# Kernel optimization log

Hardware: AMD Instinct MI355X
Metric: run time of the kernel (lower is better)

The kernel has to match this reference:

```python
import jax, jax.numpy as jnp
import numpy as np

S = 2048
HIDDEN = 4096
NH, NKV, HD = 32, 8, 128
QPK = NH // NKV  # 4
BLOCK, LOCAL, VERT = 64, 16, 8
ROPE_BASE = 1.0e6
SCALE = 1.0 / HD  # mup scaling: head_dim / mup_attn_multiplier(=1.0)


def setup_inputs() -> dict:
    key = jax.random.key(0)
    ks = jax.random.split(key, 5)
    qkv_out = NKV * (QPK + 2) * HD  # 6144, head-major layout
    return {
        "positions": jnp.arange(S, dtype=jnp.int32),
        "hidden_states": jax.random.normal(ks[0], (S, HIDDEN), jnp.float32),
        "w_qkv": jax.random.normal(ks[1], (qkv_out, HIDDEN), jnp.float32) * 0.02,
        "b_qkv": jax.random.normal(ks[2], (qkv_out,), jnp.float32) * 0.02,
        "w_dense": jax.random.normal(ks[3], (HIDDEN, HIDDEN), jnp.float32) * 0.02,
        "b_dense": jax.random.normal(ks[4], (HIDDEN,), jnp.float32) * 0.02,
    }


def _rope(x, cos, sin):
    # NeoX-style (non-interleaved) rotary over full head_dim.
    # x: [S, n_heads, HD]; cos/sin: [S, HD//2]
    d2 = x.shape[-1] // 2
    x1, x2 = x[..., :d2], x[..., d2:]
    c, s = cos[:, None, :], sin[:, None, :]
    return jnp.concatenate([x1 * c - x2 * s, x2 * c + x1 * s], axis=-1)


def _blocksparse_mask(positions):
    # vllm phi3small pattern: block (qb,kb) active iff causal AND
    # (qb-kb < local_blocks OR (kb + head + 1) % vert_stride == 0), hetero heads.
    qb = positions // BLOCK                       # [S]
    heads = jnp.arange(NH, dtype=positions.dtype)
    diff = qb[:, None] - qb[None, :]              # [S,S]
    local = diff < LOCAL                          # [S,S]
    vert = ((qb[None, None, :] + heads[:, None, None] + 1) % VERT) == 0  # [NH,1,S]
    causal = positions[:, None] >= positions[None, :]                     # [S,S]
    return (local[None] | vert) & causal[None]    # [NH,S,S]


def reference(positions, hidden_states, w_qkv, b_qkv, w_dense, b_dense):
    seq = hidden_states.shape[0]
    qkv = hidden_states @ w_qkv.T + b_qkv                   # [S, 6144]
    qkv = qkv.reshape(seq, NKV, QPK + 2, HD)                # head-major split
    q = qkv[:, :, :QPK].reshape(seq, NH, HD)
    k = qkv[:, :, QPK]                                      # [S, NKV, HD]
    v = qkv[:, :, QPK + 1]

    pos = positions.astype(jnp.float32)  # rope_position_scale = 1.0
    inv_freq = 1.0 / (ROPE_BASE ** (jnp.arange(0, HD, 2, dtype=jnp.float32) / HD))
    freqs = pos[:, None] * inv_freq                          # [S, HD/2]
    cos, sin = jnp.cos(freqs), jnp.sin(freqs)
    q = _rope(q, cos, sin)
    k = _rope(k, cos, sin)

    # GQA: each kv head serves QPK query heads
    kx = jnp.repeat(k, QPK, axis=1)                          # [S, NH, HD]
    vx = jnp.repeat(v, QPK, axis=1)

    scores = jnp.einsum('qhd,khd->hqk', q, kx) * SCALE       # [NH,S,S]
    mask = _blocksparse_mask(positions)
    scores = jnp.where(mask, scores, -jnp.inf)  # diag always in local block -> no empty rows
    p = jax.nn.softmax(scores, axis=-1)
    out = jnp.einsum('hqk,khd->qhd', p, vx).reshape(seq, NH * HD)
    return out @ w_dense.T + b_dense
```

## Files before the change

### kernel.cpp

```cpp
#include <hip/hip_runtime.h>

#define S_LEN   2048
#define HID     4096
#define NHEADS  32
#define NKVH    8
#define HDIM    128
#define NQKV    6144
#define ATT_SCALE (1.0f/128.0f)

typedef unsigned short u16;
typedef __attribute__((ext_vector_type(8))) __bf16 bf16x8;
typedef __attribute__((ext_vector_type(4))) float  f32x4;

__device__ __forceinline__ u16 f2bf(float f) {
    union { float f; unsigned u; } x; x.f = f;
    unsigned u = x.u;
    u += 0x7fffu + ((u >> 16) & 1u);
    return (u16)(u >> 16);
}
__device__ __forceinline__ float bf2f(u16 v) {
    union { unsigned u; float f; } x; x.u = ((unsigned)v) << 16; return x.f;
}

__global__ __launch_bounds__(256) void cvt_bf16_kernel(const float* __restrict__ in,
                                                       u16* __restrict__ out, int n4) {
    int stride = gridDim.x * blockDim.x;
    for (int i = blockIdx.x * blockDim.x + threadIdx.x; i < n4; i += stride) {
        float4 v = *(const float4*)(in + (size_t)i * 4);
        ushort4 o = make_ushort4(f2bf(v.x), f2bf(v.y), f2bf(v.z), f2bf(v.w));
        *(ushort4*)(out + (size_t)i * 4) = o;
    }
}

#define BM 128
#define BN 128
#define BK 32

template <bool OUT_BF16>
__global__ __launch_bounds__(256) void gemm_bt_kernel(
    const u16* __restrict__ A,
    const u16* __restrict__ B,
    const float* __restrict__ bias,
    void* __restrict__ Cout,
    int M, int N, int K)
{
    __shared__ u16 Alds[2][BM][BK];
    __shared__ u16 Blds[2][BN][BK];

    const int tid  = threadIdx.x;
    const int wid  = tid >> 6;
    const int lane = tid & 63;
    const int ln   = lane & 15;
    const int quad = lane >> 4;
    const int wm   = (wid >> 1) * 64;
    const int wn   = (wid & 1) * 64;
    const int tileM = blockIdx.y * BM;
    const int tileN = blockIdx.x * BN;

    const int srow = lane >> 2;
    const int scol = ((lane & 3) ^ ((srow >> 1) & 3)) * 8;

    f32x4 acc[4][4];
    #pragma unroll
    for (int i = 0; i < 4; i++)
        #pragma unroll
        for (int j = 0; j < 4; j++) {
            f32x4 z = {0.f, 0.f, 0.f, 0.f};
            acc[i][j] = z;
        }

    auto stage = [&](int k, int buf) {
        const int k0 = k * BK;
        #pragma unroll
        for (int p = 0; p < 2; p++) {
            int r = p * 64 + wid * 16;
            const u16* ga = A + (size_t)(tileM + r + srow) * K + k0 + scol;
            const u16* gb = B + (size_t)(tileN + r + srow) * K + k0 + scol;
            __builtin_amdgcn_global_load_lds(
                (const __attribute__((address_space(1))) void*)ga,
                (__attribute__((address_space(3))) void*)&Alds[buf][r][0], 16, 0, 0);
            __builtin_amdgcn_global_load_lds(
                (const __attribute__((address_space(1))) void*)gb,
                (__attribute__((address_space(3))) void*)&Blds[buf][r][0], 16, 0, 0);
        }
    };

    const int nIter = K / BK;
    stage(0, 0);

    const int pc = (quad ^ ((ln >> 1) & 3)) * 8;

    for (int k = 0; k < nIter; k++) {
        const int buf = k & 1;
        __syncthreads();
        if (k + 1 < nIter) stage(k + 1, buf ^ 1);

        bf16x8 af[4], bfr[4];
        #pragma unroll
        for (int i = 0; i < 4; i++)
            af[i] = *(const bf16x8*)(&Alds[buf][wm + i * 16 + ln][pc]);
        #pragma unroll
        for (int j = 0; j < 4; j++)
            bfr[j] = *(const bf16x8*)(&Blds[buf][wn + j * 16 + ln][pc]);
        #pragma unroll
        for (int i = 0; i < 4; i++)
            #pragma unroll
            for (int j = 0; j < 4; j++)
                acc[i][j] = __builtin_amdgcn_mfma_f32_16x16x32_bf16(af[i], bfr[j], acc[i][j], 0, 0, 0);
    }

    #pragma unroll
    for (int i = 0; i < 4; i++) {
        #pragma unroll
        for (int j = 0; j < 4; j++) {
            int n = tileN + wn + j * 16 + ln;
            float bv = bias[n];
            #pragma unroll
            for (int r = 0; r < 4; r++) {
                int m = tileM + wm + i * 16 + quad * 4 + r;
                float v = acc[i][j][r] + bv;
                if (OUT_BF16)
                    ((u16*)Cout)[(size_t)m * N + n] = f2bf(v);
                else
                    ((float*)Cout)[(size_t)m * N + n] = v;
            }
        }
    }
}

__global__ __launch_bounds__(128) void rope_split_kernel(
    const u16* __restrict__ qkv, const int* __restrict__ positions,
    u16* __restrict__ qb_o, u16* __restrict__ kb_o, u16* __restrict__ vb_o)
{
    const int d   = threadIdx.x;
    const int pos = blockIdx.x;
    const int hy  = blockIdx.y;
    const float p = (float)positions[pos];

    if (hy >= NHEADS + NKVH) {
        int kv = hy - NHEADS - NKVH;
        const u16* src = qkv + (size_t)pos * NQKV + (kv * 6 + 5) * HDIM;
        vb_o[((size_t)kv * S_LEN + pos) * HDIM + d] = src[d];
        return;
    }
    const u16* src;
    u16* dst;
    if (hy < NHEADS) {
        int kv = hy >> 2, qi = hy & 3;
        src = qkv + (size_t)pos * NQKV + (kv * 6 + qi) * HDIM;
        dst = qb_o + ((size_t)hy * S_LEN + pos) * HDIM;
    } else {
        int kv = hy - NHEADS;
        src = qkv + (size_t)pos * NQKV + (kv * 6 + 4) * HDIM;
        dst = kb_o + ((size_t)kv * S_LEN + pos) * HDIM;
    }
    int d2 = d & 63;
    float inv = expf(-(float)d2 * (13.815510557964274f / 64.0f));
    float fr = p * inv;
    float s, c;
    sincosf(fr, &s, &c);
    float x1 = bf2f(src[d2]);
    float x2 = bf2f(src[d2 + 64]);
    float o = (d < 64) ? (x1 * c - x2 * s) : (x2 * c + x1 * s);
    dst[d] = f2bf(o);
}

#define LDK 136
#define LDV 72
__global__ __launch_bounds__(256) void attn_bs_kernel(
    const u16* __restrict__ Q,
    const u16* __restrict__ K,
    const u16* __restrict__ V,
    u16* __restrict__ O)
{
    __shared__ u16 Qs[64][LDK];
    __shared__ u16 Ks[64][LDK];
    __shared__ u16 Vt[128][LDV];
    __shared__ u16 Ps[4][16][LDV];

    const int qb = blockIdx.x;
    const int h  = blockIdx.y;
    const int kv = h >> 2;
    const int tid  = threadIdx.x;
    const int w    = tid >> 6;
    const int lane = tid & 63;
    const int ln   = lane & 15;
    const int quad = lane >> 4;

    const u16* Qg = Q + ((size_t)h * S_LEN + qb * 64) * HDIM;
    {
        int col = (tid & 15) * 8;
        #pragma unroll
        for (int p = 0; p < 4; p++) {
            int row = p * 16 + (tid >> 4);
            *(uint4*)(&Qs[row][col]) = *(const uint4*)(Qg + row * HDIM + col);
        }
    }

    f32x4 oacc[8];
    #pragma unroll
    for (int n = 0; n < 8; n++) { f32x4 z = {0.f,0.f,0.f,0.f}; oacc[n] = z; }
    float mrow[4] = {-1e30f, -1e30f, -1e30f, -1e30f};
    float lrow[4] = {0.f, 0.f, 0.f, 0.f};

    for (int kb = 0; kb <= qb; kb++) {
        bool sel = (qb - kb < 16) || (((kb + h + 1) & 7) == 0);
        if (!sel) continue;

        __syncthreads();
        const u16* Kg = K + ((size_t)kv * S_LEN + kb * 64) * HDIM;
        const u16* Vg = V + ((size_t)kv * S_LEN + kb * 64) * HDIM;
        {
            int col = (tid & 15) * 8;
            #pragma unroll
            for (int p = 0; p < 4; p++) {
                int row = p * 16 + (tid >> 4);
                *(uint4*)(&Ks[row][col]) = *(const uint4*)(Kg + row * HDIM + col);
            }
            int key = tid & 63;
            int dbase = (tid >> 6) * 32;
            #pragma unroll
            for (int p = 0; p < 4; p++) {
                int d0 = dbase + p * 8;
                uint4 vv = *(const uint4*)(Vg + key * HDIM + d0);
                const u16* pv = (const u16*)&vv;
                #pragma unroll
                for (int jj = 0; jj < 8; jj++) Vt[d0 + jj][key] = pv[jj];
            }
        }
        __syncthreads();

        f32x4 sacc[4];
        #pragma unroll
        for (int jj = 0; jj < 4; jj++) { f32x4 z = {0.f,0.f,0.f,0.f}; sacc[jj] = z; }
        #pragma unroll
        for (int ks = 0; ks < 4; ks++) {
            bf16x8 aq = *(const bf16x8*)(&Qs[w * 16 + ln][ks * 32 + quad * 8]);
            #pragma unroll
            for (int jj = 0; jj < 4; jj++) {
                bf16x8 bk = *(const bf16x8*)(&Ks[jj * 16 + ln][ks * 32 + quad * 8]);
                sacc[jj] = __builtin_amdgcn_mfma_f32_16x16x32_bf16(aq, bk, sacc[jj], 0, 0, 0);
            }
        }

        #pragma unroll
        for (int r = 0; r < 4; r++) {
            float pv[4];
            float mx = -1e30f;
            const int qrow = w * 16 + quad * 4 + r;
            #pragma unroll
            for (int jj = 0; jj < 4; jj++) {
                float s = sacc[jj][r] * ATT_SCALE;
                if (kb == qb && (jj * 16 + ln) > qrow) s = -1e30f;
                pv[jj] = s;
                mx = fmaxf(mx, s);
            }
            #pragma unroll
            for (int off = 1; off < 16; off <<= 1)
                mx = fmaxf(mx, __shfl_xor(mx, off, 64));
            float mnew  = fmaxf(mrow[r], mx);
            float alpha = __expf(mrow[r] - mnew);
            float sum = 0.f;
            #pragma unroll
            for (int jj = 0; jj < 4; jj++) {
                float pe = __expf(pv[jj] - mnew);
                pv[jj] = pe;
                sum += pe;
            }
            #pragma unroll
            for (int off = 1; off < 16; off <<= 1)
                sum += __shfl_xor(sum, off, 64);
            lrow[r] = lrow[r] * alpha + sum;
            mrow[r] = mnew;
            #pragma unroll
            for (int n = 0; n < 8; n++) oacc[n][r] *= alpha;
            #pragma unroll
            for (int jj = 0; jj < 4; jj++)
                Ps[w][quad * 4 + r][jj * 16 + ln] = f2bf(pv[jj]);
        }
        __syncthreads();

        #pragma unroll
        for (int kk = 0; kk < 2; kk++) {
            bf16x8 ap = *(const bf16x8*)(&Ps[w][ln][kk * 32 + quad * 8]);
            #pragma unroll
            for (int n = 0; n < 8; n++) {
                bf16x8 bv = *(const bf16x8*)(&Vt[n * 16 + ln][kk * 32 + quad * 8]);
                oacc[n] = __builtin_amdgcn_mfma_f32_16x16x32_bf16(ap, bv, oacc[n], 0, 0, 0);
            }
        }
    }

    #pragma unroll
    for (int n = 0; n < 8; n++) {
        #pragma unroll
        for (int r = 0; r < 4; r++) {
            int row = w * 16 + quad * 4 + r;
            int pos = qb * 64 + row;
            float o = oacc[n][r] / lrow[r];
            O[(size_t)pos * (NHEADS * HDIM) + h * HDIM + n * 16 + ln] = f2bf(o);
        }
    }
}

extern "C" void kernel_launch(void* const* d_in, const int* in_sizes, int n_in,
                              void* d_out, int out_size, void* d_ws, size_t ws_size,
                              hipStream_t stream) {
    const int*   positions = (const int*)d_in[0];
    const float* hidden    = (const float*)d_in[1];
    const float* w_qkv     = (const float*)d_in[2];
    const float* b_qkv     = (const float*)d_in[3];
    const float* w_dense   = (const float*)d_in[4];
    const float* b_dense   = (const float*)d_in[5];
    float* out = (float*)d_out;

    char* ws = (char*)d_ws;
    u16* ws_h    = (u16*)(ws);
    u16* ws_wqkv = (u16*)(ws + 16777216);
    u16* ws_wd   = (u16*)(ws + 67108864);
    u16* ws_qkv  = (u16*)(ws + 100663296);
    u16* ws_q    = (u16*)(ws + 125829120);
    u16* ws_k    = (u16*)(ws + 142606336);
    u16* ws_v    = (u16*)(ws + 146800640);
    u16* ws_attn = (u16*)(ws + 150994944);

    cvt_bf16_kernel<<<1024, 256, 0, stream>>>(hidden,  ws_h,    (S_LEN * HID) / 4);
    cvt_bf16_kernel<<<2048, 256, 0, stream>>>(w_qkv,   ws_wqkv, (NQKV * HID) / 4);
    cvt_bf16_kernel<<<2048, 256, 0, stream>>>(w_dense, ws_wd,   (HID * HID) / 4);

    gemm_bt_kernel<true><<<dim3(NQKV / BN, S_LEN / BM), 256, 0, stream>>>(
        ws_h, ws_wqkv, b_qkv, ws_qkv, S_LEN, NQKV, HID);

    rope_split_kernel<<<dim3(S_LEN, NHEADS + 2 * NKVH), 128, 0, stream>>>(
        ws_qkv, positions, ws_q, ws_k, ws_v);

    attn_bs_kernel<<<dim3(S_LEN / 64, NHEADS), 256, 0, stream>>>(ws_q, ws_k, ws_v, ws_attn);

    gemm_bt_kernel<false><<<dim3(HID / BN, S_LEN / BM), 256, 0, stream>>>(
        ws_attn, ws_wd, b_dense, out, S_LEN, HID, HID);
}
```

Baseline: 576.6 us.

## Swizzle attention LDS layouts, load K via direct-to-LDS, keep Q in registers

Reworks the block-sparse attention kernel. The padded LDS arrays become XOR-swizzled layouts, K tiles are loaded with global_load_lds straight into shared memory, and Q fragments are held in registers instead of LDS. The block order is reversed so the heaviest query blocks start first, and MFMA sections get raised wave priority. The block-level barrier before the PV stage is dropped because each wave only reads its own P slice, and launch bounds request four blocks per CU. This targets LDS bank conflicts, LDS capacity, load latency and tail imbalance, at the cost of more register pressure and subtle ordering assumptions around the wave-private P buffer.

```diff
diff --git a/kernel.cpp b/kernel.cpp
--- a/kernel.cpp
+++ b/kernel.cpp
@@ -165,20 +165,17 @@
     dst[d] = f2bf(o);
 }
 
-#define LDK 136
-#define LDV 72
-__global__ __launch_bounds__(256) void attn_bs_kernel(
+__global__ __launch_bounds__(256, 4) void attn_bs_kernel(
     const u16* __restrict__ Q,
     const u16* __restrict__ K,
     const u16* __restrict__ V,
     u16* __restrict__ O)
 {
-    __shared__ u16 Qs[64][LDK];
-    __shared__ u16 Ks[64][LDK];
-    __shared__ u16 Vt[128][LDV];
-    __shared__ u16 Ps[4][16][LDV];
-
-    const int qb = blockIdx.x;
+    __shared__ u16 Ks[64 * 128];
+    __shared__ u16 Vt[128 * 64];
+    __shared__ u16 Ps[4][16 * 64];
+
+    const int qb = (int)gridDim.x - 1 - (int)blockIdx.x;
     const int h  = blockIdx.y;
     const int kv = h >> 2;
     const int tid  = threadIdx.x;
@@ -187,14 +184,12 @@
     const int ln   = lane & 15;
     const int quad = lane >> 4;
 
-    const u16* Qg = Q + ((size_t)h * S_LEN + qb * 64) * HDIM;
+    bf16x8 aq[4];
     {
-        int col = (tid & 15) * 8;
-        #pragma unroll
-        for (int p = 0; p < 4; p++) {
-            int row = p * 16 + (tid >> 4);
-            *(uint4*)(&Qs[row][col]) = *(const uint4*)(Qg + row * HDIM + col);
-        }
+        const u16* Qg = Q + ((size_t)h * S_LEN + qb * 64 + w * 16 + ln) * HDIM + quad * 8;
+        #pragma unroll
+        for (int ks = 0; ks < 4; ks++)
+            aq[ks] = *(const bf16x8*)(Qg + ks * 32);
     }
 
     f32x4 oacc[8];
@@ -208,24 +203,32 @@
         if (!sel) continue;
 
         __syncthreads();
+
         const u16* Kg = K + ((size_t)kv * S_LEN + kb * 64) * HDIM;
         const u16* Vg = V + ((size_t)kv * S_LEN + kb * 64) * HDIM;
+
+        #pragma unroll
+        for (int p = 0; p < 4; p++) {
+            int r0  = w * 16 + p * 4;
+            int row = r0 + (lane >> 4);
+            const u16* src = Kg + (size_t)row * HDIM + (((lane & 15) ^ (row & 7)) << 3);
+            __builtin_amdgcn_global_load_lds(
+                (const __attribute__((address_space(1))) void*)src,
+                (__attribute__((address_space(3))) void*)&Ks[r0 * 128], 16, 0, 0);
+        }
+
         {
-            int col = (tid & 15) * 8;
-            #pragma unroll
-            for (int p = 0; p < 4; p++) {
-                int row = p * 16 + (tid >> 4);
-                *(uint4*)(&Ks[row][col]) = *(const uint4*)(Kg + row * HDIM + col);
-            }
-            int key = tid & 63;
-            int dbase = (tid >> 6) * 32;
+            int dbase = w * 32;
             #pragma unroll
             for (int p = 0; p < 4; p++) {
                 int d0 = dbase + p * 8;
-                uint4 vv = *(const uint4*)(Vg + key * HDIM + d0);
-                const u16* pv = (const u16*)&vv;
+                uint4 vv = *(const uint4*)(Vg + (size_t)lane * HDIM + d0);
+                const u16* pvv = (const u16*)&vv;
                 #pragma unroll
-                for (int jj = 0; jj < 8; jj++) Vt[d0 + jj][key] = pv[jj];
+                for (int jj = 0; jj < 8; jj++) {
+                    int d = d0 + jj;
+                    Vt[d * 64 + ((((lane >> 3)) ^ (d & 7)) << 3) + (lane & 7)] = pvv[jj];
+                }
             }
         }
         __syncthreads();
@@ -233,15 +236,17 @@
         f32x4 sacc[4];
         #pragma unroll
         for (int jj = 0; jj < 4; jj++) { f32x4 z = {0.f,0.f,0.f,0.f}; sacc[jj] = z; }
+        __builtin_amdgcn_s_setprio(1);
         #pragma unroll
         for (int ks = 0; ks < 4; ks++) {
-            bf16x8 aq = *(const bf16x8*)(&Qs[w * 16 + ln][ks * 32 + quad * 8]);
             #pragma unroll
             for (int jj = 0; jj < 4; jj++) {
-                bf16x8 bk = *(const bf16x8*)(&Ks[jj * 16 + ln][ks * 32 + quad * 8]);
-                sacc[jj] = __builtin_amdgcn_mfma_f32_16x16x32_bf16(aq, bk, sacc[jj], 0, 0, 0);
-            }
-        }
+                bf16x8 bk = *(const bf16x8*)(
+                    &Ks[(jj * 16 + ln) * 128 + (((ks * 4 + quad) ^ (ln & 7)) << 3)]);
+                sacc[jj] = __builtin_amdgcn_mfma_f32_16x16x32_bf16(aq[ks], bk, sacc[jj], 0, 0, 0);
+            }
+        }
+        __builtin_amdgcn_s_setprio(0);
 
         #pragma unroll
         for (int r = 0; r < 4; r++) {
@@ -274,21 +279,26 @@
             mrow[r] = mnew;
             #pragma unroll
             for (int n = 0; n < 8; n++) oacc[n][r] *= alpha;
+            const int prow = quad * 4 + r;
             #pragma unroll
             for (int jj = 0; jj < 4; jj++)
-                Ps[w][quad * 4 + r][jj * 16 + ln] = f2bf(pv[jj]);
-        }
-        __syncthreads();
-
+                Ps[w][prow * 64 + (((jj * 2 + (ln >> 3)) ^ (prow & 7)) << 3) + (ln & 7)]
+                    = f2bf(pv[jj]);
+        }
+
+        __builtin_amdgcn_s_setprio(1);
         #pragma unroll
         for (int kk = 0; kk < 2; kk++) {
-            bf16x8 ap = *(const bf16x8*)(&Ps[w][ln][kk * 32 + quad * 8]);
+            bf16x8 ap = *(const bf16x8*)(
+                &Ps[w][ln * 64 + (((kk * 4 + quad) ^ (ln & 7)) << 3)]);
             #pragma unroll
             for (int n = 0; n < 8; n++) {
-                bf16x8 bv = *(const bf16x8*)(&Vt[n * 16 + ln][kk * 32 + quad * 8]);
+                bf16x8 bv = *(const bf16x8*)(
+                    &Vt[(n * 16 + ln) * 64 + (((kk * 4 + quad) ^ (ln & 7)) << 3)]);
                 oacc[n] = __builtin_amdgcn_mfma_f32_16x16x32_bf16(ap, bv, oacc[n], 0, 0, 0);
             }
         }
+        __builtin_amdgcn_s_setprio(0);
     }
 
     #pragma unroll
```

After: 565.6 us. About the same (-1.9%).
